# Kernel optimization log

Hardware: AMD Instinct MI355X
Metric: run time of the kernel (lower is better)

## Reference

```python
import jax, jax.numpy as jnp
import numpy as np

N_NODES = 100000
N_EDGES = 1600000
D_IN = 128
D_HID = 128
N_GRAPHS = 128


def setup_inputs() -> dict:
    key = jax.random.key(0)
    ks = jax.random.split(key, 6)
    x = jax.random.normal(ks[0], (N_NODES, D_IN), dtype=jnp.float32)
    edge_index = jax.random.randint(ks[1], (2, N_EDGES), 0, N_NODES, dtype=jnp.int32)
    batch = jnp.sort(jax.random.randint(ks[2], (N_NODES,), 0, N_GRAPHS, dtype=jnp.int32))
    # GCNConv params (glorot-ish weight, zero bias), PReLU slope init 0.25 per channel
    W = jax.random.normal(ks[3], (D_IN, D_HID), dtype=jnp.float32) / np.float32(np.sqrt(D_IN))
    b = jnp.zeros((D_HID,), dtype=jnp.float32)
    prelu_a = jnp.full((D_HID,), 0.25, dtype=jnp.float32)
    return {"x": x, "edge_index": edge_index, "batch": batch, "W": W, "b": b, "prelu_a": prelu_a}


def reference(x, edge_index, batch, W, b, prelu_a):
    n_nodes = x.shape[0]
    # ---- GCNConv: add self-loops, symmetric deg^-1/2 normalization ----
    h = x @ W  # [N, H]
    loop = jnp.arange(n_nodes, dtype=edge_index.dtype)
    src = jnp.concatenate([edge_index[0], loop])  # [E+N]
    dst = jnp.concatenate([edge_index[1], loop])
    deg = jax.ops.segment_sum(jnp.ones_like(dst, jnp.float32), dst, num_segments=n_nodes)
    dinv = jnp.where(deg > 0, jax.lax.rsqrt(deg), 0.0)  # deg^-1/2 (inf -> 0, as in PyG)
    norm = dinv[src] * dinv[dst]  # [E+N]
    msg = h[src] * norm[:, None]  # gather + scale
    out = jax.ops.segment_sum(msg, dst, num_segments=n_nodes) + b  # scatter-add
    # ---- PReLU (per-channel slope) ----
    out = jnp.where(out > 0, out, prelu_a * out)
    # ---- F.normalize: L2 over dim=1, eps=1e-12 ----
    nrm = jnp.sqrt(jnp.sum(out * out, axis=1, keepdims=True))
    out = out / jnp.maximum(nrm, 1e-12)
    # ---- global_mean_pool over batch ids ----
    cnt = jax.ops.segment_sum(jnp.ones((n_nodes,), jnp.float32), batch, num_segments=N_GRAPHS)
    pooled = jax.ops.segment_sum(out, batch, num_segments=N_GRAPHS) / jnp.maximum(cnt, 1.0)[:, None]
    return pooled  # [N_GRAPHS, D_HID]
```

## Files before the change

### kernel.cpp

```cpp
#include <hip/hip_runtime.h>

#define D 128
#define NG 128
#define CAP 64
#define BIN 128
#define EPB 4096
#define NBMAX 1024

typedef unsigned short ushort_t;
typedef __bf16 bf16x8 __attribute__((ext_vector_type(8)));
typedef float floatx4 __attribute__((ext_vector_type(4)));

static __device__ __forceinline__ unsigned short f2bf(float f) {
    unsigned u = __float_as_uint(f);
    unsigned r = (u + 0x7fffu + ((u >> 16) & 1u)) >> 16;
    return (unsigned short)r;
}
static __device__ __forceinline__ float bflo(unsigned v) { return __uint_as_float(v << 16); }
static __device__ __forceinline__ float bfhi(unsigned v) { return __uint_as_float(v & 0xffff0000u); }

__global__ __launch_bounds__(256) void k_init(const float* __restrict__ W, ushort_t* __restrict__ Wp,
                                              const int* __restrict__ batch, int N,
                                              float* __restrict__ cntinv, float* __restrict__ out,
                                              int* __restrict__ cursor, int nb, int cap) {
    int t = blockIdx.x * 256 + threadIdx.x;
    int T = gridDim.x * 256;
    for (int i = t; i < NG * D; i += T) out[i] = 0.f;
    for (int b = t; b < nb; b += T) cursor[b] = b * cap;
    if (blockIdx.x == 0) {
        int tid = threadIdx.x;
        for (int i = tid; i < D * D; i += 256) {
            int c = i >> 7, k = i & 127;
            Wp[i] = f2bf(W[k * D + c]);
        }
        if (tid < NG) {
            int g = tid;
            int lo = 0, hi = N;
            while (lo < hi) { int mid = (lo + hi) >> 1; if (batch[mid] < g) lo = mid + 1; else hi = mid; }
            int a = lo;
            hi = N;
            while (lo < hi) { int mid = (lo + hi) >> 1; if (batch[mid] < g + 1) lo = mid + 1; else hi = mid; }
            int c = lo - a;
            cntinv[g] = 1.0f / (float)(c > 1 ? c : 1);
        }
    }
}

__global__ __launch_bounds__(256) void k_ascatter(const int* __restrict__ src, const int* __restrict__ dst,
                                                  int E, int nb, int* __restrict__ cursor,
                                                  int* __restrict__ ebuf) {
    __shared__ int hist[NBMAX];
    __shared__ int curs[NBMAX];
    int tid = threadIdx.x;
    for (int i = tid; i < nb; i += 256) hist[i] = 0;
    __syncthreads();
    int base = blockIdx.x * EPB;
    int cnt = E - base; if (cnt > EPB) cnt = EPB;
    for (int k = tid; k < cnt; k += 256) {
        atomicAdd(&hist[(unsigned)dst[base + k] >> 7], 1);
    }
    __syncthreads();
    for (int i = tid; i < nb; i += 256) {
        int v = hist[i];
        curs[i] = v ? atomicAdd(&cursor[i], v) : 0;
    }
    __syncthreads();
    for (int k = tid; k < cnt; k += 256) {
        int dv = dst[base + k];
        int sv = src[base + k];
        int pos = atomicAdd(&curs[dv >> 7], 1);
        ebuf[pos] = sv | ((dv & 127) << 24);
    }
}

__global__ __launch_bounds__(256) void k_bucketpad(const int* __restrict__ ebuf, const int* __restrict__ cursor,
                                                   int cap, int N, int* __restrict__ deg,
                                                   int* __restrict__ elist) {
    __shared__ int lists[BIN * CAP];
    __shared__ int lcnt[BIN];
    int tid = threadIdx.x;
    int b = blockIdx.x;
    for (int i = tid; i < BIN; i += 256) lcnt[i] = 0;
    __syncthreads();
    int s = b * cap;
    int e = cursor[b];
    for (int i = s + tid; i < e; i += 256) {
        int pk = ebuf[i];
        int n = (unsigned)pk >> 24;
        int pos = atomicAdd(&lcnt[n], 1);
        if (pos < CAP) lists[n * CAP + pos] = pk & 0xFFFFFF;
    }
    __syncthreads();
    int n0 = b * BIN;
    for (int i = tid; i < BIN; i += 256) {
        int node = n0 + i;
        if (node < N) deg[node] = min(lcnt[i], CAP);
    }
    int4* dp = (int4*)(elist + (size_t)n0 * CAP);
    const int4* sp = (const int4*)lists;
#pragma unroll
    for (int i = tid; i < BIN * CAP / 4; i += 256) dp[i] = sp[i];
}

__global__ __launch_bounds__(256) void k_gemm(const float* __restrict__ x, const ushort_t* __restrict__ Wp,
                                              const int* __restrict__ deg, ushort_t* __restrict__ h, int N) {
    __shared__ ushort_t smem[64 * 132 + 128 * 128];
    ushort_t* xs = smem;
    ushort_t* ws = smem + 64 * 132;

    const int tid = threadIdx.x;
    const int w = tid >> 6;
    const int lane = tid & 63;
    const int q = lane >> 4;
    const int m = lane & 15;
    const int row0 = blockIdx.x * 64;

#pragma unroll
    for (int it = 0; it < 8; ++it) {
        int i = it * 256 + tid;
        int r = i >> 5, s = i & 31;
        int row = row0 + r;
        uint2 pk;
        if (row < N) {
            float4 v = *(const float4*)&x[(size_t)row * D + s * 4];
            pk.x = (unsigned)f2bf(v.x) | ((unsigned)f2bf(v.y) << 16);
            pk.y = (unsigned)f2bf(v.z) | ((unsigned)f2bf(v.w) << 16);
        } else {
            pk.x = 0; pk.y = 0;
        }
        int off = (s * 8) ^ ((r & 7) << 4);
        *(uint2*)((char*)xs + r * 256 + off) = pk;
    }
#pragma unroll
    for (int it = 0; it < 8; ++it) {
        int i = it * 256 + tid;
        int c = i >> 4, s = i & 15;
        bf16x8 v = *(const bf16x8*)(Wp + (size_t)c * D + s * 8);
        int off = (s * 16) ^ ((c & 7) << 4);
        *(bf16x8*)((char*)ws + c * 256 + off) = v;
    }
    __syncthreads();

    floatx4 acc[8];
#pragma unroll
    for (int nt = 0; nt < 8; ++nt) acc[nt] = (floatx4){0.f, 0.f, 0.f, 0.f};

    const int arow_l = w * 16 + m;
    const int swz = (m & 7) << 4;
#pragma unroll
    for (int kb = 0; kb < 4; ++kb) {
        const int koff = (kb * 64 + q * 16) ^ swz;
        const bf16x8 av = *(const bf16x8*)((const char*)xs + arow_l * 256 + koff);
#pragma unroll
        for (int nt = 0; nt < 8; ++nt) {
            int c = nt * 16 + m;
            const bf16x8 bv = *(const bf16x8*)((const char*)ws + c * 256 + koff);
            acc[nt] = __builtin_amdgcn_mfma_f32_16x16x32_bf16(av, bv, acc[nt], 0, 0, 0);
        }
    }

    float di[4];
#pragma unroll
    for (int r = 0; r < 4; ++r) {
        int row = row0 + w * 16 + q * 4 + r;
        di[r] = (row < N) ? rsqrtf((float)(deg[row] + 1)) : 0.f;
    }
    __syncthreads();

#pragma unroll
    for (int nt = 0; nt < 8; ++nt) {
#pragma unroll
        for (int r = 0; r < 4; ++r) {
            xs[(w * 16 + q * 4 + r) * 132 + nt * 16 + m] = f2bf(acc[nt][r] * di[r]);
        }
    }
    __syncthreads();
#pragma unroll
    for (int it = 0; it < 8; ++it) {
        int i = it * 256 + tid;
        int r = i >> 5, s = i & 31;
        int row = row0 + r;
        if (row < N) {
            *(uint2*)&h[(size_t)row * D + s * 4] = *(const uint2*)&xs[r * 132 + s * 4];
        }
    }
}

__global__ __launch_bounds__(256) void k_gather(const ushort_t* __restrict__ h,
                                                const int* __restrict__ deg, const int* __restrict__ elist,
                                                const int* __restrict__ batch, const float* __restrict__ b,
                                                const float* __restrict__ pa, const float* __restrict__ cntinv,
                                                float* __restrict__ out, int N) {
    __shared__ float rows[4][128];
    __shared__ int gids[4];
    const int wave = threadIdx.x >> 6;
    const int lane = threadIdx.x & 63;
    const int half = lane >> 5;
    const int fl = lane & 31;
    const int node = blockIdx.x * 4 + wave;
    const int nodeC = (node < N) ? node : (N - 1);
    const bool valid = (node < N);

    float a0 = 0.f, a1 = 0.f, a2 = 0.f, a3 = 0.f;

    size_t start = (size_t)nodeC * CAP;
    int len = valid ? deg[nodeC] : 0;
    {
        int m = len;
        int idx = (lane < len) ? elist[start + lane] : 0;
        int j = 0;
        for (; j + 8 <= m; j += 8) {
            int i0 = __shfl(idx, j + half);
            int i1 = __shfl(idx, j + 2 + half);
            int i2 = __shfl(idx, j + 4 + half);
            int i3 = __shfl(idx, j + 6 + half);
            uint2 v0 = *(const uint2*)&h[(size_t)i0 * D + fl * 4];
            uint2 v1 = *(const uint2*)&h[(size_t)i1 * D + fl * 4];
            uint2 v2 = *(const uint2*)&h[(size_t)i2 * D + fl * 4];
            uint2 v3 = *(const uint2*)&h[(size_t)i3 * D + fl * 4];
            a0 += bflo(v0.x); a1 += bfhi(v0.x); a2 += bflo(v0.y); a3 += bfhi(v0.y);
            a0 += bflo(v1.x); a1 += bfhi(v1.x); a2 += bflo(v1.y); a3 += bfhi(v1.y);
            a0 += bflo(v2.x); a1 += bfhi(v2.x); a2 += bflo(v2.y); a3 += bfhi(v2.y);
            a0 += bflo(v3.x); a1 += bfhi(v3.x); a2 += bflo(v3.y); a3 += bfhi(v3.y);
        }
        for (; j + 2 <= m; j += 2) {
            int i0 = __shfl(idx, j + half);
            uint2 v0 = *(const uint2*)&h[(size_t)i0 * D + fl * 4];
            a0 += bflo(v0.x); a1 += bfhi(v0.x); a2 += bflo(v0.y); a3 += bfhi(v0.y);
        }
        if (j < m) {
            int i0 = __shfl(idx, j);
            if (half == 0) {
                uint2 v0 = *(const uint2*)&h[(size_t)i0 * D + fl * 4];
                a0 += bflo(v0.x); a1 += bfhi(v0.x); a2 += bflo(v0.y); a3 += bfhi(v0.y);
            }
        }
    }

    a0 += __shfl_xor(a0, 32);
    a1 += __shfl_xor(a1, 32);
    a2 += __shfl_xor(a2, 32);
    a3 += __shfl_xor(a3, 32);

    uint2 sv = *(const uint2*)&h[(size_t)nodeC * D + fl * 4];
    a0 += bflo(sv.x); a1 += bfhi(sv.x); a2 += bflo(sv.y); a3 += bfhi(sv.y);

    float dinv = rsqrtf((float)(len + 1));
    float4 bb = *(const float4*)&b[fl * 4];
    float4 aa = *(const float4*)&pa[fl * 4];
    float v0 = a0 * dinv + bb.x;
    float v1 = a1 * dinv + bb.y;
    float v2 = a2 * dinv + bb.z;
    float v3 = a3 * dinv + bb.w;
    v0 = v0 > 0.f ? v0 : aa.x * v0;
    v1 = v1 > 0.f ? v1 : aa.y * v1;
    v2 = v2 > 0.f ? v2 : aa.z * v2;
    v3 = v3 > 0.f ? v3 : aa.w * v3;
    float ss = v0 * v0 + v1 * v1 + v2 * v2 + v3 * v3;
#pragma unroll
    for (int o = 16; o > 0; o >>= 1) ss += __shfl_xor(ss, o);
    float inv = valid ? (1.0f / fmaxf(sqrtf(ss), 1e-12f)) : 0.f;

    if (half == 0) {
        *(float4*)&rows[wave][fl * 4] = make_float4(v0 * inv, v1 * inv, v2 * inv, v3 * inv);
        if (fl == 0) gids[wave] = batch[nodeC];
    }
    __syncthreads();

    if (threadIdx.x < 128) {
        int f = threadIdx.x;
        float acc = rows[0][f];
        int g = gids[0];
#pragma unroll
        for (int i = 1; i < 4; ++i) {
            int gi = gids[i];
            float vv = rows[i][f];
            if (gi == g) {
                acc += vv;
            } else {
                atomicAdd(&out[(size_t)g * D + f], acc * cntinv[g]);
                g = gi;
                acc = vv;
            }
        }
        atomicAdd(&out[(size_t)g * D + f], acc * cntinv[g]);
    }
}

extern "C" void kernel_launch(void* const* d_in, const int* in_sizes, int n_in,
                              void* d_out, int out_size, void* d_ws, size_t ws_size,
                              hipStream_t stream) {
    const float* x = (const float*)d_in[0];
    const int* ei = (const int*)d_in[1];
    const int* batch = (const int*)d_in[2];
    const float* W = (const float*)d_in[3];
    const float* b = (const float*)d_in[4];
    const float* pa = (const float*)d_in[5];
    float* out = (float*)d_out;

    const int N = in_sizes[0] / D;
    const int E = in_sizes[1] / 2;
    const int* src = ei;
    const int* dst = ei + E;

    const int nb = (N + BIN - 1) / BIN;
    const int nblk = (E + EPB - 1) / EPB;
    const int mean = (E + nb - 1) / nb;
    const int cap = mean + mean / 5 + 512;

    char* w = (char*)d_ws;
    auto carve = [&](size_t bytes) {
        void* p = (void*)w;
        w += (bytes + 255) & ~(size_t)255;
        return p;
    };
    char* hbase = (char*)carve((size_t)N * D * sizeof(ushort_t));
    ushort_t* h = (ushort_t*)hbase;
    int* ebuf = (int*)hbase;
    ushort_t* Wp = (ushort_t*)carve((size_t)D * D * sizeof(ushort_t));
    int* deg = (int*)carve((size_t)N * sizeof(int));
    int* elist = (int*)carve((size_t)nb * BIN * CAP * sizeof(int));
    int* cursor = (int*)carve(NBMAX * sizeof(int));
    float* cntinv = (float*)carve(NG * sizeof(float));

    k_init<<<32, 256, 0, stream>>>(W, Wp, batch, N, cntinv, out, cursor, nb, cap);
    k_ascatter<<<nblk, 256, 0, stream>>>(src, dst, E, nb, cursor, ebuf);
    k_bucketpad<<<nb, 256, 0, stream>>>(ebuf, cursor, cap, N, deg, elist);
    k_gemm<<<(N + 63) / 64, 256, 0, stream>>>(x, Wp, deg, h, N);
    k_gather<<<(N + 3) / 4, 256, 0, stream>>>(h, deg, elist, batch, b, pa, cntinv, out, N);
}
```

Baseline: 240.4 us.

## Compact per-node edge lists in place and store precomputed byte offsets

The bucket kernel now writes each node's neighbor list compactly back into the edge buffer, using a shared-memory prefix scan to find row starts. This replaces the padded 64-slot-per-node elist array, which cuts the bytes written by the bucket step and read by the gather step. Source indices are stored as byte offsets into h (src*256), so the gather loop needs only an add per load. Edges per scatter block are doubled, and h is no longer aliased with the edge buffer, which costs some extra workspace.

Measured after the change: 244.4 us. No clear change (+1.6%).

```diff
diff --git a/kernel.cpp b/kernel.cpp
--- a/kernel.cpp
+++ b/kernel.cpp
@@ -4,7 +4,7 @@
 #define NG 128
 #define CAP 64
 #define BIN 128
-#define EPB 4096
+#define EPB 8192
 #define NBMAX 1024
 
 typedef unsigned short ushort_t;
@@ -18,6 +18,10 @@
 }
 static __device__ __forceinline__ float bflo(unsigned v) { return __uint_as_float(v << 16); }
 static __device__ __forceinline__ float bfhi(unsigned v) { return __uint_as_float(v & 0xffff0000u); }
+static __device__ __forceinline__ void acc2(float2& a, unsigned v) {
+    a.x += __uint_as_float(v << 16);
+    a.y += __uint_as_float(v & 0xffff0000u);
+}
 
 __global__ __launch_bounds__(256) void k_init(const float* __restrict__ W, ushort_t* __restrict__ Wp,
                                               const int* __restrict__ batch, int N,
@@ -69,15 +73,15 @@
         int dv = dst[base + k];
         int sv = src[base + k];
         int pos = atomicAdd(&curs[dv >> 7], 1);
-        ebuf[pos] = sv | ((dv & 127) << 24);
-    }
-}
-
-__global__ __launch_bounds__(256) void k_bucketpad(const int* __restrict__ ebuf, const int* __restrict__ cursor,
-                                                   int cap, int N, int* __restrict__ deg,
-                                                   int* __restrict__ elist) {
+        ebuf[pos] = (sv << 7) | ((dv & 127) << 24);
+    }
+}
+
+__global__ __launch_bounds__(256) void k_bucket(int* __restrict__ ebuf, const int* __restrict__ cursor,
+                                                int cap, int N, int* __restrict__ rs, int* __restrict__ deg) {
     __shared__ int lists[BIN * CAP];
     __shared__ int lcnt[BIN];
+    __shared__ int lpos[BIN];
     int tid = threadIdx.x;
     int b = blockIdx.x;
     for (int i = tid; i < BIN; i += 256) lcnt[i] = 0;
@@ -91,15 +95,28 @@
         if (pos < CAP) lists[n * CAP + pos] = pk & 0xFFFFFF;
     }
     __syncthreads();
+    int c0 = (tid < BIN) ? min(lcnt[tid], CAP) : 0;
+    if (tid < BIN) lpos[tid] = c0;
+    __syncthreads();
+    for (int off = 1; off < BIN; off <<= 1) {
+        int tv = 0;
+        if (tid < BIN && tid >= off) tv = lpos[tid - off];
+        __syncthreads();
+        if (tid < BIN) lpos[tid] += tv;
+        __syncthreads();
+    }
     int n0 = b * BIN;
-    for (int i = tid; i < BIN; i += 256) {
-        int node = n0 + i;
-        if (node < N) deg[node] = min(lcnt[i], CAP);
-    }
-    int4* dp = (int4*)(elist + (size_t)n0 * CAP);
-    const int4* sp = (const int4*)lists;
-#pragma unroll
-    for (int i = tid; i < BIN * CAP / 4; i += 256) dp[i] = sp[i];
+    if (tid < BIN) {
+        int node = n0 + tid;
+        if (node < N) { rs[node] = s + lpos[tid] - c0; deg[node] = c0; }
+    }
+    __syncthreads();
+    {
+        int n = tid >> 1, hf = tid & 1;
+        int c = min(lcnt[n], CAP);
+        int wbase = s + lpos[n] - c;
+        for (int k = hf; k < c; k += 2) ebuf[wbase + k] = lists[n * CAP + k] << 1;
+    }
 }
 
 __global__ __launch_bounds__(256) void k_gemm(const float* __restrict__ x, const ushort_t* __restrict__ Wp,
@@ -187,7 +204,8 @@
 }
 
 __global__ __launch_bounds__(256) void k_gather(const ushort_t* __restrict__ h,
-                                                const int* __restrict__ deg, const int* __restrict__ elist,
+                                                const int* __restrict__ rs, const int* __restrict__ deg,
+                                                const int* __restrict__ ebuf,
                                                 const int* __restrict__ batch, const float* __restrict__ b,
                                                 const float* __restrict__ pa, const float* __restrict__ cntinv,
                                                 float* __restrict__ out, int N) {
@@ -200,58 +218,60 @@
     const int node = blockIdx.x * 4 + wave;
     const int nodeC = (node < N) ? node : (N - 1);
     const bool valid = (node < N);
-
-    float a0 = 0.f, a1 = 0.f, a2 = 0.f, a3 = 0.f;
-
-    size_t start = (size_t)nodeC * CAP;
+    const char* hb = (const char*)h;
+    const unsigned flb = (unsigned)fl * 8;
+
+    float2 a01 = {0.f, 0.f}, a23 = {0.f, 0.f};
+
+    int start = valid ? rs[nodeC] : 0;
     int len = valid ? deg[nodeC] : 0;
     {
         int m = len;
-        int idx = (lane < len) ? elist[start + lane] : 0;
+        int idx = (lane < len) ? ebuf[start + lane] : 0;
         int j = 0;
         for (; j + 8 <= m; j += 8) {
-            int i0 = __shfl(idx, j + half);
-            int i1 = __shfl(idx, j + 2 + half);
-            int i2 = __shfl(idx, j + 4 + half);
-            int i3 = __shfl(idx, j + 6 + half);
-            uint2 v0 = *(const uint2*)&h[(size_t)i0 * D + fl * 4];
-            uint2 v1 = *(const uint2*)&h[(size_t)i1 * D + fl * 4];
-            uint2 v2 = *(const uint2*)&h[(size_t)i2 * D + fl * 4];
-            uint2 v3 = *(const uint2*)&h[(size_t)i3 * D + fl * 4];
-            a0 += bflo(v0.x); a1 += bfhi(v0.x); a2 += bflo(v0.y); a3 += bfhi(v0.y);
-            a0 += bflo(v1.x); a1 += bfhi(v1.x); a2 += bflo(v1.y); a3 += bfhi(v1.y);
-            a0 += bflo(v2.x); a1 += bfhi(v2.x); a2 += bflo(v2.y); a3 += bfhi(v2.y);
-            a0 += bflo(v3.x); a1 += bfhi(v3.x); a2 += bflo(v3.y); a3 += bfhi(v3.y);
+            unsigned o0 = (unsigned)__shfl(idx, j + half) + flb;
+            unsigned o1 = (unsigned)__shfl(idx, j + 2 + half) + flb;
+            unsigned o2 = (unsigned)__shfl(idx, j + 4 + half) + flb;
+            unsigned o3 = (unsigned)__shfl(idx, j + 6 + half) + flb;
+            uint2 v0 = *(const uint2*)(hb + o0);
+            uint2 v1 = *(const uint2*)(hb + o1);
+            uint2 v2 = *(const uint2*)(hb + o2);
+            uint2 v3 = *(const uint2*)(hb + o3);
+            acc2(a01, v0.x); acc2(a23, v0.y);
+            acc2(a01, v1.x); acc2(a23, v1.y);
+            acc2(a01, v2.x); acc2(a23, v2.y);
+            acc2(a01, v3.x); acc2(a23, v3.y);
         }
         for (; j + 2 <= m; j += 2) {
-            int i0 = __shfl(idx, j + half);
-            uint2 v0 = *(const uint2*)&h[(size_t)i0 * D + fl * 4];
-            a0 += bflo(v0.x); a1 += bfhi(v0.x); a2 += bflo(v0.y); a3 += bfhi(v0.y);
+            unsigned o0 = (unsigned)__shfl(idx, j + half) + flb;
+            uint2 v0 = *(const uint2*)(hb + o0);
+            acc2(a01, v0.x); acc2(a23, v0.y);
         }
         if (j < m) {
-            int i0 = __shfl(idx, j);
+            unsigned o0 = (unsigned)__shfl(idx, j) + flb;
             if (half == 0) {
-                uint2 v0 = *(const uint2*)&h[(size_t)i0 * D + fl * 4];
-                a0 += bflo(v0.x); a1 += bfhi(v0.x); a2 += bflo(v0.y); a3 += bfhi(v0.y);
+                uint2 v0 = *(const uint2*)(hb + o0);
+                acc2(a01, v0.x); acc2(a23, v0.y);
             }
         }
     }
 
-    a0 += __shfl_xor(a0, 32);
-    a1 += __shfl_xor(a1, 32);
-    a2 += __shfl_xor(a2, 32);
-    a3 += __shfl_xor(a3, 32);
+    a01.x += __shfl_xor(a01.x, 32);
+    a01.y += __shfl_xor(a01.y, 32);
+    a23.x += __shfl_xor(a23.x, 32);
+    a23.y += __shfl_xor(a23.y, 32);
 
     uint2 sv = *(const uint2*)&h[(size_t)nodeC * D + fl * 4];
-    a0 += bflo(sv.x); a1 += bfhi(sv.x); a2 += bflo(sv.y); a3 += bfhi(sv.y);
+    acc2(a01, sv.x); acc2(a23, sv.y);
 
     float dinv = rsqrtf((float)(len + 1));
     float4 bb = *(const float4*)&b[fl * 4];
     float4 aa = *(const float4*)&pa[fl * 4];
-    float v0 = a0 * dinv + bb.x;
-    float v1 = a1 * dinv + bb.y;
-    float v2 = a2 * dinv + bb.z;
-    float v3 = a3 * dinv + bb.w;
+    float v0 = a01.x * dinv + bb.x;
+    float v1 = a01.y * dinv + bb.y;
+    float v2 = a23.x * dinv + bb.z;
+    float v3 = a23.y * dinv + bb.w;
     v0 = v0 > 0.f ? v0 : aa.x * v0;
     v1 = v1 > 0.f ? v1 : aa.y * v1;
     v2 = v2 > 0.f ? v2 : aa.z * v2;
@@ -314,18 +334,17 @@
         w += (bytes + 255) & ~(size_t)255;
         return p;
     };
-    char* hbase = (char*)carve((size_t)N * D * sizeof(ushort_t));
-    ushort_t* h = (ushort_t*)hbase;
-    int* ebuf = (int*)hbase;
+    ushort_t* h = (ushort_t*)carve((size_t)N * D * sizeof(ushort_t));
     ushort_t* Wp = (ushort_t*)carve((size_t)D * D * sizeof(ushort_t));
     int* deg = (int*)carve((size_t)N * sizeof(int));
-    int* elist = (int*)carve((size_t)nb * BIN * CAP * sizeof(int));
+    int* rs = (int*)carve((size_t)N * sizeof(int));
+    int* ebuf = (int*)carve((size_t)nb * cap * sizeof(int));
     int* cursor = (int*)carve(NBMAX * sizeof(int));
     float* cntinv = (float*)carve(NG * sizeof(float));
 
     k_init<<<32, 256, 0, stream>>>(W, Wp, batch, N, cntinv, out, cursor, nb, cap);
     k_ascatter<<<nblk, 256, 0, stream>>>(src, dst, E, nb, cursor, ebuf);
-    k_bucketpad<<<nb, 256, 0, stream>>>(ebuf, cursor, cap, N, deg, elist);
+    k_bucket<<<nb, 256, 0, stream>>>(ebuf, cursor, cap, N, rs, deg);
     k_gemm<<<(N + 63) / 64, 256, 0, stream>>>(x, Wp, deg, h, N);
-    k_gather<<<(N + 3) / 4, 256, 0, stream>>>(h, deg, elist, batch, b, pa, cntinv, out, N);
-}
+    k_gather<<<(N + 3) / 4, 256, 0, stream>>>(h, rs, deg, ebuf, batch, b, pa, cntinv, out, N);
+}
```
